# Kernel optimization log

Hardware: AMD Instinct MI355X
Metric: run time of the kernel (lower is better)

## Reference

```python
import jax, jax.numpy as jnp
import numpy as np

E = 128
H = 4
D = E // H  # head dim = 32
NEG = -1e9


def setup_inputs() -> dict:
    key = jax.random.key(0)
    ks = jax.random.split(key, 4)
    B, N = 8, 2048
    x = jax.random.normal(ks[0], (B, N, E), dtype=jnp.float32)
    adj = jax.random.randint(ks[1], (B, N, N), 0, 2, dtype=jnp.int32)
    # nn.MultiheadAttention params: packed in_proj (3E,E) + out_proj (E,E)
    in_proj_w = jax.random.normal(ks[2], (3 * E, E), dtype=jnp.float32) * (1.0 / np.sqrt(E))
    in_proj_b = jnp.zeros((3 * E,), dtype=jnp.float32)
    out_w = jax.random.normal(ks[3], (E, E), dtype=jnp.float32) * (1.0 / np.sqrt(E))
    out_b = jnp.zeros((E,), dtype=jnp.float32)
    return {"x": x, "adj": adj, "in_proj_w": in_proj_w, "in_proj_b": in_proj_b,
            "out_w": out_w, "out_b": out_b}


def reference(x, adj, in_proj_w, in_proj_b, out_w, out_b):
    B, N, _ = x.shape
    # additive mask from FIRST batch element only (as in the torch module)
    mask = jnp.where(adj[0] == 0, jnp.float32(NEG), jnp.float32(0.0))  # (N,N)
    # packed QKV projection: x @ W^T + b
    qkv = x @ in_proj_w.T + in_proj_b  # (B,N,3E)
    q, k, v = jnp.split(qkv, 3, axis=-1)
    # (B,N,E) -> (B,H,N,D)
    def heads(t):
        return t.reshape(B, N, H, D).transpose(0, 2, 1, 3)
    q, k, v = heads(q), heads(k), heads(v)
    scores = jnp.einsum('bhnd,bhmd->bhnm', q, k) / jnp.sqrt(jnp.float32(D))
    scores = scores + mask[None, None]  # broadcast shared mask
    attn = jax.nn.softmax(scores, axis=-1)
    out = jnp.einsum('bhnm,bhmd->bhnd', attn, v)  # (B,H,N,D)
    out = out.transpose(0, 2, 1, 3).reshape(B, N, E)
    return out @ out_w.T + out_b
```

## Files before the change

kernel.cpp:

```cpp
#include <hip/hip_runtime.h>


#define EDIM 128
#define SCALE2 0.25503483f
#define COFF  -5.7707801f

typedef unsigned int uint32;
typedef float f32x4 __attribute__((ext_vector_type(4)));
typedef short s16x8 __attribute__((ext_vector_type(8)));
typedef _Float16 f16x2 __attribute__((ext_vector_type(2)));
typedef _Float16 f16x4 __attribute__((ext_vector_type(4)));
typedef _Float16 f16x8 __attribute__((ext_vector_type(8)));
typedef __fp16 g16x2 __attribute__((ext_vector_type(2)));

__device__ inline float bf2f(ushort u) { return __uint_as_float(((uint32)u) << 16); }
__device__ inline ushort f2bf(float f) {
  uint32 u = __float_as_uint(f);
  u += 0x7fffu + ((u >> 16) & 1u);
  return (ushort)(u >> 16);
}
__device__ inline uint32 packbf(float a, float b) {
  uint32 ua = __float_as_uint(a) + 0x8000u;
  uint32 ub = __float_as_uint(b) + 0x8000u;
  return __builtin_amdgcn_perm(ub, ua, 0x07060302u);
}
__device__ inline f16x2 pkrtz(float a, float b) {
  g16x2 t = __builtin_amdgcn_cvt_pkrtz(a, b);
  return __builtin_bit_cast(f16x2, t);
}
__device__ inline float fexp2(float x) {
#if __has_builtin(__builtin_amdgcn_exp2f)
  return __builtin_amdgcn_exp2f(x);
#else
  return __exp2f(x);
#endif
}

__device__ inline f32x4 mfma32(s16x8 a, s16x8 b, f32x4 c) {
  return __builtin_amdgcn_mfma_f32_16x16x32_bf16(a, b, c, 0, 0, 0);
}
__device__ inline f32x4 mfma32h(f16x8 a, f16x8 b, f32x4 c) {
  return __builtin_amdgcn_mfma_f32_16x16x32_f16(a, b, c, 0, 0, 0);
}

__device__ inline int sniff_fp32(const ushort* __restrict__ xus) {
  int lane = threadIdx.x & 63, cnt = 0;
#pragma unroll
  for (int i = 0; i < 4; i++) {
    ushort v = xus[2 * (lane * 4 + i)];
    int ex = (v >> 7) & 0xFF;
    cnt += (ex >= 100 && ex <= 140) ? 1 : 0;
  }
#pragma unroll
  for (int s = 1; s < 64; s <<= 1) cnt += __shfl_xor(cnt, s);
  return cnt < 128;
}

__device__ inline s16x8 load8(const void* p, size_t e, int fp32) {
  if (fp32) {
    const float* f = (const float*)p + e;
    float4 lo = *(const float4*)f;
    float4 hi = *(const float4*)(f + 4);
    union { s16x8 s; uint32 u[4]; } r;
    r.u[0] = packbf(lo.x, lo.y);
    r.u[1] = packbf(lo.z, lo.w);
    r.u[2] = packbf(hi.x, hi.y);
    r.u[3] = packbf(hi.z, hi.w);
    return r.s;
  }
  return *(const s16x8*)((const ushort*)p + e);
}
__device__ inline float loads(const void* p, size_t e, int fp32) {
  return fp32 ? ((const float*)p)[e] : bf2f(((const ushort*)p)[e]);
}

__global__ __launch_bounds__(256) void k_pre(const void* __restrict__ x,
                                             const void* __restrict__ w,
                                             const void* __restrict__ bias,
                                             ushort* __restrict__ Qg,
                                             ushort* __restrict__ Kg,
                                             _Float16* __restrict__ Vth,
                                             const int4* __restrict__ adj4,
                                             uint32* __restrict__ mb) {
  if (blockIdx.y >= 6) {
    int g = ((blockIdx.y - 6) * 256 + blockIdx.x) * 256 + threadIdx.x;
    int4 v = adj4[g];
    int lane = threadIdx.x & 63;
    uint32 nib = (v.x != 0 ? 1u : 0u) | (v.y != 0 ? 2u : 0u) |
                 (v.z != 0 ? 4u : 0u) | (v.w != 0 ? 8u : 0u);
    uint32 wbit = nib << (4 * (lane & 7));
    wbit |= __shfl_xor(wbit, 1);
    wbit |= __shfl_xor(wbit, 2);
    wbit |= __shfl_xor(wbit, 4);
    if ((lane & 7) == 0) mb[g >> 3] = wbit;
    return;
  }

  const int fp32 = sniff_fp32((const ushort*)x);
  const int tid = threadIdx.x;
  const int wave = tid >> 6, lane = tid & 63, L = lane & 15, quad = lane >> 4;
  const int mt = blockIdx.x * 64 + wave * 16;
  const int jt0 = blockIdx.y * 4;

  s16x8 a[4];
#pragma unroll
  for (int ks = 0; ks < 4; ks++)
    a[ks] = load8(x, (size_t)(mt + L) * EDIM + ks * 32 + quad * 8, fp32);

  const int bidx = mt >> 11;
  const int npos0 = (mt & 2047) + quad * 4;

  for (int jj = 0; jj < 4; jj++) {
    int jt = jt0 + jj;
    f32x4 acc = {0.f, 0.f, 0.f, 0.f};
#pragma unroll
    for (int ks = 0; ks < 4; ks++) {
      s16x8 bf = load8(w, (size_t)(jt * 16 + L) * EDIM + ks * 32 + quad * 8, fp32);
      acc = mfma32(a[ks], bf, acc);
    }
    int j = jt * 16 + L;
    float badd = loads(bias, j, fp32);
    int jm = j & 127;
    int h = jm >> 5, d = jm & 31;
    int bh = bidx * 4 + h;
    int ch = npos0 >> 7, kk = npos0 & 127;
    if (jt < 8) {
#pragma unroll
      for (int r = 0; r < 4; r++)
        Qg[(size_t)bh * 65536 + (size_t)(npos0 + r) * 32 + d] = f2bf((acc[r] + badd) * SCALE2);
    } else if (jt < 16) {
      int sub = kk >> 5, k32 = kk & 31, t = k32 >> 3, r8 = k32 & 7;
      int slot0 = sub * 32 + ((r8 >> 2) << 4) + t * 4;
      size_t kb = (size_t)bh * 65536 + (size_t)ch * 4096;
#pragma unroll
      for (int r = 0; r < 4; r++)
        Kg[kb + (size_t)(slot0 + r) * 32 + (((d >> 3) ^ r) << 3) + (d & 7)] =
            f2bf(acc[r] + badd);
    } else {
      int g = kk >> 3, e0 = kk & 7;
      f16x2 h0 = pkrtz(acc[0] + badd, acc[1] + badd);
      f16x2 h1 = pkrtz(acc[2] + badd, acc[3] + badd);
      f16x4 pk; pk[0] = h0[0]; pk[1] = h0[1]; pk[2] = h1[0]; pk[3] = h1[1];
      *(f16x4*)(Vth + (size_t)bh * 65536 + (size_t)ch * 4096 + d * 128 +
                (g ^ (d & 7)) * 8 + e0) = pk;
    }
  }
}

__global__ __launch_bounds__(512, 8) void k_attn(const ushort* __restrict__ Qg,
                                                 const ushort* __restrict__ Kg,
                                                 const _Float16* __restrict__ Vth,
                                                 const uint32* __restrict__ mb,
                                                 ushort* __restrict__ Oa) {
  __shared__ float cb[2176];

  const int tid = threadIdx.x;
  const int wv = tid >> 6, lane = tid & 63, L = lane & 15, quad = lane >> 4;
  const int half = wv >> 2, wl = wv & 3;
  const int bid = blockIdx.x;
  const int bh = ((bid >> 3) & 3) * 8 + (bid & 7);
  const int qc = bid >> 5;
  const int q0 = qc * 64 + wl * 16;
  const int qgA = q0 + L;

  const ushort* Qb = Qg + (size_t)bh * 65536;
  s16x8 qfA = *(const s16x8*)(Qb + (size_t)qgA * 32 + quad * 8);

  f32x4 OA0 = {0,0,0,0}, OA1 = {0,0,0,0}, LA = {0,0,0,0};
  f16x8 ones;
#pragma unroll
  for (int i = 0; i < 8; i++) ones[i] = (_Float16)1.0f;

  const char* Kg8 = (const char*)(Kg + (size_t)bh * 65536) + (size_t)half * 65536;
  const char* Vg8 = (const char*)(Vth + (size_t)bh * 65536) + (size_t)half * 65536;
  const int g0 = quad ^ (L & 3);

  const char* kA = Kg8 + L * 64 + g0 * 16;
  const char* vA = Vg8 + L * 256;
  const uint32* mbA = mb + (size_t)qgA * 64 + half * 32;

#define MW4(M, S) ((S) == 0 ? (M).x : (S) == 1 ? (M).y : (S) == 2 ? (M).z : (M).w)

#pragma unroll
  for (int cc = 0; cc < 8; cc++) {
    uint4 mA = *(const uint4*)(mbA + cc * 4);
    const char* kc = kA + cc * 8192;
    const char* vc = vA + cc * 8192;
#pragma unroll
    for (int sub = 0; sub < 4; sub++) {
      const f32x4 Zc = {COFF, COFF, COFF, COFF};
      s16x8 kf0 = *(const s16x8*)(kc + sub * 2048);
      s16x8 kf1 = *(const s16x8*)(kc + sub * 2048 + 1024);
      f32x4 sA0 = mfma32(kf0, qfA, Zc), sA1 = mfma32(kf1, qfA, Zc);

      uint32 mwqA = MW4(mA, sub) >> (quad * 8);
      union { f16x8 v; f16x2 h[4]; } pA;
      float a0 = ((mwqA >> 0) & 1u) ? fexp2(sA0[0]) : 0.f;
      float a1 = ((mwqA >> 1) & 1u) ? fexp2(sA0[1]) : 0.f;
      float a2 = ((mwqA >> 2) & 1u) ? fexp2(sA0[2]) : 0.f;
      float a3 = ((mwqA >> 3) & 1u) ? fexp2(sA0[3]) : 0.f;
      float a4 = ((mwqA >> 4) & 1u) ? fexp2(sA1[0]) : 0.f;
      float a5 = ((mwqA >> 5) & 1u) ? fexp2(sA1[1]) : 0.f;
      float a6 = ((mwqA >> 6) & 1u) ? fexp2(sA1[2]) : 0.f;
      float a7 = ((mwqA >> 7) & 1u) ? fexp2(sA1[3]) : 0.f;
      pA.h[0] = pkrtz(a0, a1); pA.h[1] = pkrtz(a2, a3);
      pA.h[2] = pkrtz(a4, a5); pA.h[3] = pkrtz(a6, a7);

      int vg = (sub * 4 + quad) ^ (L & 7);
      f16x8 vf0 = *(const f16x8*)(vc + vg * 16);
      f16x8 vf1 = *(const f16x8*)(vc + 4096 + vg * 16);
      OA0 = mfma32h(vf0, pA.v, OA0);
      OA1 = mfma32h(vf1, pA.v, OA1);
      LA  = mfma32h(ones, pA.v, LA);
    }
  }
#undef MW4

  __syncthreads();
  const int cbase = wl * 544;
  if (half) {
#pragma unroll
    for (int r = 0; r < 4; r++) {
      cb[cbase + L * 33 + quad * 4 + r]      = OA0[r];
      cb[cbase + L * 33 + 16 + quad * 4 + r] = OA1[r];
    }
    if (quad == 0) cb[cbase + 528 + L] = LA[0];
  }
  __syncthreads();
  if (!half) {
#pragma unroll
    for (int r = 0; r < 4; r++) {
      OA0[r] += cb[cbase + L * 33 + quad * 4 + r];
      OA1[r] += cb[cbase + L * 33 + 16 + quad * 4 + r];
    }
    float rn = 1.0f / (LA[0] + cb[cbase + 528 + L]);
    int b = bh >> 2, h = bh & 3;
    size_t ob = ((size_t)(b * 2048 + qgA)) * 128 + h * 32 + quad * 4;
    ushort4 p0, p1;
    p0.x = f2bf(OA0[0] * rn); p0.y = f2bf(OA0[1] * rn);
    p0.z = f2bf(OA0[2] * rn); p0.w = f2bf(OA0[3] * rn);
    p1.x = f2bf(OA1[0] * rn); p1.y = f2bf(OA1[1] * rn);
    p1.z = f2bf(OA1[2] * rn); p1.w = f2bf(OA1[3] * rn);
    *(ushort4*)(Oa + ob) = p0; *(ushort4*)(Oa + ob + 16) = p1;
  }
}

__global__ __launch_bounds__(256) void k_proj(void* outp, const ushort* Oa,
                                              const void* w, const void* bias,
                                              const ushort* __restrict__ xus) {
  const int fp32 = sniff_fp32(xus);
  const ushort* src = Oa;
  const int tid = threadIdx.x;
  const int wave = tid >> 6, lane = tid & 63, L = lane & 15, quad = lane >> 4;
  const int mt = blockIdx.x * 64 + wave * 16;
  const int jt0 = blockIdx.y * 2;

  s16x8 a[4];
#pragma unroll
  for (int ks = 0; ks < 4; ks++)
    a[ks] = *(const s16x8*)(src + (size_t)(mt + L) * EDIM + ks * 32 + quad * 8);

  for (int jt = jt0; jt < jt0 + 2; jt++) {
    f32x4 acc = {0.f, 0.f, 0.f, 0.f};
#pragma unroll
    for (int ks = 0; ks < 4; ks++) {
      s16x8 bf = load8(w, (size_t)(jt * 16 + L) * EDIM + ks * 32 + quad * 8, fp32);
      acc = mfma32(a[ks], bf, acc);
    }
    float badd = loads(bias, jt * 16 + L, fp32);
#pragma unroll
    for (int r = 0; r < 4; r++) {
      size_t idx = (size_t)(mt + quad * 4 + r) * EDIM + jt * 16 + L;
      if (fp32) ((float*)outp)[idx] = acc[r] + badd;
      else      ((ushort*)outp)[idx] = f2bf(acc[r] + badd);
    }
  }
}

extern "C" void kernel_launch(void* const* d_in, const int* in_sizes, int n_in,
                              void* d_out, int out_size, void* d_ws, size_t ws_size,
                              hipStream_t stream) {
  const void* x   = d_in[0];
  const int*  adj = (const int*)d_in[1];
  const void* ipw = d_in[2];
  const void* ipb = d_in[3];
  const void* ow  = d_in[4];
  const void* ob  = d_in[5];

  char* ws = (char*)d_ws;
  ushort*   Qg  = (ushort*)(ws);
  ushort*   Kg  = (ushort*)(ws + ((size_t)4 << 20));
  _Float16* Vth = (_Float16*)(ws + ((size_t)8 << 20));
  uint32*   mb  = (uint32*)(ws + ((size_t)12 << 20));
  ushort*   Oa  = (ushort*)(ws + ((size_t)13 << 20));

  hipLaunchKernelGGL(k_pre, dim3(256, 22), dim3(256), 0, stream, x, ipw, ipb,
                     Qg, Kg, Vth, (const int4*)adj, mb);
  hipLaunchKernelGGL(k_attn, dim3(1024), dim3(512), 0, stream, Qg, Kg, Vth, mb,
                     Oa);
  hipLaunchKernelGGL(k_proj, dim3(256, 4), dim3(256), 0, stream, d_out, Oa, ow, ob,
                     (const ushort*)x);
}
```

Measured before the change: 258.7 us.

## Process four query tiles per wave and split keys four ways across waves

Each wave now holds four 16-row query tiles and reuses every loaded K/V fragment across all four, cutting K/V global load traffic per unit of compute. The key range is split into quarters across wave groups, with a larger LDS reduction combining partial outputs and row sums from three peer waves. The grid is halved to 512 blocks and the launch-bounds occupancy hint is lowered to 4. This trades higher register pressure, more LDS and fewer blocks for better data reuse.

```diff
diff --git a/kernel.cpp b/kernel.cpp
--- a/kernel.cpp
+++ b/kernel.cpp
@@ -147,100 +147,126 @@
   }
 }
 
-__global__ __launch_bounds__(512, 8) void k_attn(const ushort* __restrict__ Qg,
+__global__ __launch_bounds__(512, 4) void k_attn(const ushort* __restrict__ Qg,
                                                  const ushort* __restrict__ Kg,
                                                  const _Float16* __restrict__ Vth,
                                                  const uint32* __restrict__ mb,
                                                  ushort* __restrict__ Oa) {
-  __shared__ float cb[2176];
+  __shared__ float cb[13056];
 
   const int tid = threadIdx.x;
   const int wv = tid >> 6, lane = tid & 63, L = lane & 15, quad = lane >> 4;
-  const int half = wv >> 2, wl = wv & 3;
+  const int wl = wv & 1, qt = wv >> 1;
   const int bid = blockIdx.x;
   const int bh = ((bid >> 3) & 3) * 8 + (bid & 7);
   const int qc = bid >> 5;
-  const int q0 = qc * 64 + wl * 16;
-  const int qgA = q0 + L;
+  const int q0 = qc * 128 + wl * 64;
 
   const ushort* Qb = Qg + (size_t)bh * 65536;
-  s16x8 qfA = *(const s16x8*)(Qb + (size_t)qgA * 32 + quad * 8);
-
-  f32x4 OA0 = {0,0,0,0}, OA1 = {0,0,0,0}, LA = {0,0,0,0};
+  s16x8 qf[4];
+#pragma unroll
+  for (int t = 0; t < 4; t++)
+    qf[t] = *(const s16x8*)(Qb + (size_t)(q0 + t * 16 + L) * 32 + quad * 8);
+
+  f32x4 OA0[4], OA1[4], LA[4];
+#pragma unroll
+  for (int t = 0; t < 4; t++) {
+    OA0[t] = (f32x4){0, 0, 0, 0};
+    OA1[t] = (f32x4){0, 0, 0, 0};
+    LA[t]  = (f32x4){0, 0, 0, 0};
+  }
   f16x8 ones;
 #pragma unroll
   for (int i = 0; i < 8; i++) ones[i] = (_Float16)1.0f;
 
-  const char* Kg8 = (const char*)(Kg + (size_t)bh * 65536) + (size_t)half * 65536;
-  const char* Vg8 = (const char*)(Vth + (size_t)bh * 65536) + (size_t)half * 65536;
+  const char* Kg8 = (const char*)(Kg + (size_t)bh * 65536) + (size_t)qt * 32768;
+  const char* Vg8 = (const char*)(Vth + (size_t)bh * 65536) + (size_t)qt * 32768;
   const int g0 = quad ^ (L & 3);
 
   const char* kA = Kg8 + L * 64 + g0 * 16;
   const char* vA = Vg8 + L * 256;
-  const uint32* mbA = mb + (size_t)qgA * 64 + half * 32;
 
 #define MW4(M, S) ((S) == 0 ? (M).x : (S) == 1 ? (M).y : (S) == 2 ? (M).z : (M).w)
 
 #pragma unroll
-  for (int cc = 0; cc < 8; cc++) {
-    uint4 mA = *(const uint4*)(mbA + cc * 4);
+  for (int cc = 0; cc < 4; cc++) {
+    uint4 mA[4];
+#pragma unroll
+    for (int t = 0; t < 4; t++)
+      mA[t] = *(const uint4*)(mb + (size_t)(q0 + t * 16 + L) * 64 + qt * 16 + cc * 4);
     const char* kc = kA + cc * 8192;
     const char* vc = vA + cc * 8192;
+
 #pragma unroll
     for (int sub = 0; sub < 4; sub++) {
-      const f32x4 Zc = {COFF, COFF, COFF, COFF};
       s16x8 kf0 = *(const s16x8*)(kc + sub * 2048);
       s16x8 kf1 = *(const s16x8*)(kc + sub * 2048 + 1024);
-      f32x4 sA0 = mfma32(kf0, qfA, Zc), sA1 = mfma32(kf1, qfA, Zc);
-
-      uint32 mwqA = MW4(mA, sub) >> (quad * 8);
-      union { f16x8 v; f16x2 h[4]; } pA;
-      float a0 = ((mwqA >> 0) & 1u) ? fexp2(sA0[0]) : 0.f;
-      float a1 = ((mwqA >> 1) & 1u) ? fexp2(sA0[1]) : 0.f;
-      float a2 = ((mwqA >> 2) & 1u) ? fexp2(sA0[2]) : 0.f;
-      float a3 = ((mwqA >> 3) & 1u) ? fexp2(sA0[3]) : 0.f;
-      float a4 = ((mwqA >> 4) & 1u) ? fexp2(sA1[0]) : 0.f;
-      float a5 = ((mwqA >> 5) & 1u) ? fexp2(sA1[1]) : 0.f;
-      float a6 = ((mwqA >> 6) & 1u) ? fexp2(sA1[2]) : 0.f;
-      float a7 = ((mwqA >> 7) & 1u) ? fexp2(sA1[3]) : 0.f;
-      pA.h[0] = pkrtz(a0, a1); pA.h[1] = pkrtz(a2, a3);
-      pA.h[2] = pkrtz(a4, a5); pA.h[3] = pkrtz(a6, a7);
-
       int vg = (sub * 4 + quad) ^ (L & 7);
       f16x8 vf0 = *(const f16x8*)(vc + vg * 16);
       f16x8 vf1 = *(const f16x8*)(vc + 4096 + vg * 16);
-      OA0 = mfma32h(vf0, pA.v, OA0);
-      OA1 = mfma32h(vf1, pA.v, OA1);
-      LA  = mfma32h(ones, pA.v, LA);
+
+#pragma unroll
+      for (int t = 0; t < 4; t++) {
+        const f32x4 Zc = {COFF, COFF, COFF, COFF};
+        f32x4 sA0 = mfma32(kf0, qf[t], Zc), sA1 = mfma32(kf1, qf[t], Zc);
+
+        uint32 mwq = MW4(mA[t], sub) >> (quad * 8);
+        union { f16x8 v; f16x2 h[4]; } pA;
+        float a0 = ((mwq >> 0) & 1u) ? fexp2(sA0[0]) : 0.f;
+        float a1 = ((mwq >> 1) & 1u) ? fexp2(sA0[1]) : 0.f;
+        float a2 = ((mwq >> 2) & 1u) ? fexp2(sA0[2]) : 0.f;
+        float a3 = ((mwq >> 3) & 1u) ? fexp2(sA0[3]) : 0.f;
+        float a4 = ((mwq >> 4) & 1u) ? fexp2(sA1[0]) : 0.f;
+        float a5 = ((mwq >> 5) & 1u) ? fexp2(sA1[1]) : 0.f;
+        float a6 = ((mwq >> 6) & 1u) ? fexp2(sA1[2]) : 0.f;
+        float a7 = ((mwq >> 7) & 1u) ? fexp2(sA1[3]) : 0.f;
+        pA.h[0] = pkrtz(a0, a1); pA.h[1] = pkrtz(a2, a3);
+        pA.h[2] = pkrtz(a4, a5); pA.h[3] = pkrtz(a6, a7);
+
+        OA0[t] = mfma32h(vf0, pA.v, OA0[t]);
+        OA1[t] = mfma32h(vf1, pA.v, OA1[t]);
+        LA[t]  = mfma32h(ones, pA.v, LA[t]);
+      }
     }
   }
 #undef MW4
 
   __syncthreads();
-  const int cbase = wl * 544;
-  if (half) {
+#pragma unroll
+  for (int t = 0; t < 4; t++) {
+    if (t == qt) continue;
+    int widx = qt - (qt > t ? 1 : 0);
+    int base = ((wl * 4 + t) * 3 + widx) * 544;
 #pragma unroll
     for (int r = 0; r < 4; r++) {
-      cb[cbase + L * 33 + quad * 4 + r]      = OA0[r];
-      cb[cbase + L * 33 + 16 + quad * 4 + r] = OA1[r];
-    }
-    if (quad == 0) cb[cbase + 528 + L] = LA[0];
+      cb[base + L * 33 + quad * 4 + r]      = OA0[t][r];
+      cb[base + L * 33 + 16 + quad * 4 + r] = OA1[t][r];
+    }
+    if (quad == 0) cb[base + 528 + L] = LA[t][0];
   }
   __syncthreads();
-  if (!half) {
-#pragma unroll
-    for (int r = 0; r < 4; r++) {
-      OA0[r] += cb[cbase + L * 33 + quad * 4 + r];
-      OA1[r] += cb[cbase + L * 33 + 16 + quad * 4 + r];
-    }
-    float rn = 1.0f / (LA[0] + cb[cbase + 528 + L]);
+#pragma unroll
+  for (int t = 0; t < 4; t++) {
+    if (t != qt) continue;
+    float lsum = LA[t][0];
+#pragma unroll
+    for (int s = 0; s < 3; s++) {
+      int base = ((wl * 4 + t) * 3 + s) * 544;
+#pragma unroll
+      for (int r = 0; r < 4; r++) {
+        OA0[t][r] += cb[base + L * 33 + quad * 4 + r];
+        OA1[t][r] += cb[base + L * 33 + 16 + quad * 4 + r];
+      }
+      lsum += cb[base + 528 + L];
+    }
+    float rn = 1.0f / lsum;
     int b = bh >> 2, h = bh & 3;
-    size_t ob = ((size_t)(b * 2048 + qgA)) * 128 + h * 32 + quad * 4;
+    size_t ob = ((size_t)(b * 2048 + q0 + t * 16 + L)) * 128 + h * 32 + quad * 4;
     ushort4 p0, p1;
-    p0.x = f2bf(OA0[0] * rn); p0.y = f2bf(OA0[1] * rn);
-    p0.z = f2bf(OA0[2] * rn); p0.w = f2bf(OA0[3] * rn);
-    p1.x = f2bf(OA1[0] * rn); p1.y = f2bf(OA1[1] * rn);
-    p1.z = f2bf(OA1[2] * rn); p1.w = f2bf(OA1[3] * rn);
+    p0.x = f2bf(OA0[t][0] * rn); p0.y = f2bf(OA0[t][1] * rn);
+    p0.z = f2bf(OA0[t][2] * rn); p0.w = f2bf(OA0[t][3] * rn);
+    p1.x = f2bf(OA1[t][0] * rn); p1.y = f2bf(OA1[t][1] * rn);
+    p1.z = f2bf(OA1[t][2] * rn); p1.w = f2bf(OA1[t][3] * rn);
     *(ushort4*)(Oa + ob) = p0; *(ushort4*)(Oa + ob + 16) = p1;
   }
 }
@@ -296,7 +322,7 @@
 
   hipLaunchKernelGGL(k_pre, dim3(256, 22), dim3(256), 0, stream, x, ipw, ipb,
                      Qg, Kg, Vth, (const int4*)adj, mb);
-  hipLaunchKernelGGL(k_attn, dim3(1024), dim3(512), 0, stream, Qg, Kg, Vth, mb,
+  hipLaunchKernelGGL(k_attn, dim3(512), dim3(512), 0, stream, Qg, Kg, Vth, mb,
                      Oa);
   hipLaunchKernelGGL(k_proj, dim3(256, 4), dim3(256), 0, stream, d_out, Oa, ow, ob,
                      (const ushort*)x);
```

Result: slower. 287.8 us (+11.2%).
